# Kernel optimization log

Measured on AMD Instinct MI355X. Metric: run time of the kernel, lower is better.

Reference implementation:

```python
import jax, jax.numpy as jnp
import numpy as np

B, T, C, H, W = 16, 8, 2048, 16, 8
C8, C4, HW, NP = C // 8, C // 4, H * W, T // 2


def _cbr(x, w, s, b):
    # 1x1 conv + folded BN (eval-mode affine) + ReLU; x: (N, Cin, H, W), w: (Cout, Cin)
    y = jnp.einsum('oc,nchw->nohw', w, x)
    return jax.nn.relu(y * s[None, :, None, None] + b[None, :, None, None])


def setup_inputs():
    key = jax.random.key(0)
    ks = jax.random.split(key, 16)
    r = lambda i, shape, sc: jax.random.normal(ks[i], shape, jnp.float32) * sc
    return dict(
        featmap=r(0, (B, T, C, H, W), 1.0),
        re_featmap=r(1, (B * T, C, H, W), 1.0),
        vect_featmap=r(2, (B, T, C), 1.0),
        embed_feat=r(3, (B, T, 128, H, W), 1.0),
        gamma_w=r(4, (C8, C), 0.03), gamma_s=jnp.ones((C8,)), gamma_b=jnp.zeros((C8,)),
        beta_w=r(5, (C8, C), 0.03), beta_s=jnp.ones((C8,)), beta_b=jnp.zeros((C8,)),
        gg_w=r(6, (128, 2 * HW), 0.05), gg_s=jnp.ones((128,)), gg_b=jnp.zeros((128,)),
        tte_w=r(7, (128, 256), 0.05), tte_s=jnp.ones((128,)), tte_b=jnp.zeros((128,)),
        te_w=r(8, (1, 256), 0.05), te_s=jnp.ones((1,)), te_b=jnp.zeros((1,)),
        theta_w=r(9, (C8, C), 0.03), theta_b=jnp.zeros((C8,)),
        cp_w1=r(10, (C8, C4), 0.05), cp_b1=jnp.zeros((C8,)),
        cp_w2=r(11, (C, C8), 0.05), cp_b2=jnp.zeros((C,)),
    )


def reference(featmap, re_featmap, vect_featmap, embed_feat,
              gamma_w, gamma_s, gamma_b, beta_w, beta_s, beta_b,
              gg_w, gg_s, gg_b, tte_w, tte_s, tte_b, te_w, te_s, te_b,
              theta_w, theta_b, cp_w1, cp_b1, cp_w2, cp_b2):
    # spatial attention embeddings: (B, T, C8, HW)
    gamma = _cbr(re_featmap, gamma_w, gamma_s, gamma_b).reshape(B, T, C8, HW)
    beta = _cbr(re_featmap, beta_w, beta_s, beta_b).reshape(B, T, C8, HW)

    # channel attention: Conv1d over time of (B, C, T) -> (B, C8, T)
    cp = jax.nn.relu(jnp.einsum('oc,btc->bot', theta_w, vect_featmap) + theta_b[None, :, None])
    cp = cp.reshape(B, C8, NP, 2)
    c0 = cp[..., 0].transpose(0, 2, 1)  # (B, NP, C8)
    c1 = cp[..., 1].transpose(0, 2, 1)

    def mlp(x):  # (B, NP, C4) -> sigmoid gate (B, NP, C)
        h1 = jax.nn.relu(x @ cp_w1.T + cp_b1)
        return jax.nn.sigmoid(h1 @ cp_w2.T + cp_b2)

    p00 = mlp(jnp.concatenate([c0, c1], -1))  # (B, NP, C)
    p01 = mlp(jnp.concatenate([c1, c0], -1))

    # pairwise spatial graphs
    g0, g1 = gamma[:, 0::2], gamma[:, 1::2]  # (B, NP, C8, HW)
    b0, b1 = beta[:, 0::2], beta[:, 1::2]
    Gs0 = jnp.einsum('bpcs,bpct->bpst', g0, b1)  # (B, NP, HW, HW)
    Gs1 = jnp.einsum('bpcs,bpct->bpst', g1, b0)
    # Gs_in = Gs^T viewed as (HW, H, W); Gs_out = Gs viewed likewise
    j0 = jnp.concatenate([Gs0.transpose(0, 1, 3, 2), Gs1], 2).reshape(B * NP, 2 * HW, H, W)
    j1 = jnp.concatenate([Gs1.transpose(0, 1, 3, 2), Gs0], 2).reshape(B * NP, 2 * HW, H, W)
    gj0 = _cbr(j0, gg_w, gg_s, gg_b)  # (B*NP, 128, H, W)
    gj1 = _cbr(j1, gg_w, gg_s, gg_b)

    ef = embed_feat.reshape(B, NP, 2, 128, H, W)
    e0 = ef[:, :, 0].reshape(B * NP, 128, H, W)
    e1 = ef[:, :, 1].reshape(B * NP, 128, H, W)
    ta = _cbr(jnp.concatenate([e0, e1], 1), tte_w, tte_s, tte_b)  # (B*NP, 128, H, W)
    tb = _cbr(jnp.concatenate([e1, e0], 1), tte_w, tte_s, tte_b)

    def gate(t_feat, gj):  # conv 256->1 + BN + sigmoid
        y = jnp.einsum('oc,nchw->nohw', te_w, jnp.concatenate([t_feat, gj], 1))
        return jax.nn.sigmoid(y * te_s[None, :, None, None] + te_b[None, :, None, None])

    pa = gate(ta, gj0).reshape(B, NP, 1, H, W)
    pb = gate(tb, gj1).reshape(B, NP, 1, H, W)

    f = featmap.reshape(B, NP, 2, C, H, W)
    gate0 = p00[..., None, None] * pa  # (B, NP, C, H, W)
    gate1 = p01[..., None, None] * pb
    out = jax.nn.relu(gate0 * f[:, :, 0] + gate1 * f[:, :, 1])
    return out * out  # (B, T//2, C, H, W)
```

## Files before the change

### kernel.cpp

```cpp
#include <hip/hip_runtime.h>
#include <stdint.h>


typedef _Float16 f16;
typedef _Float16 f16x4 __attribute__((ext_vector_type(4)));
typedef _Float16 f16x8 __attribute__((ext_vector_type(8)));
typedef float f32x4 __attribute__((ext_vector_type(4)));

typedef const void __attribute__((address_space(1)))* gptr1;
typedef void __attribute__((address_space(3)))* lptr3;

__device__ __forceinline__ void gload16(const void* g, void* l) {
  __builtin_amdgcn_global_load_lds((gptr1)g, (lptr3)l, 16, 0, 0);
}

__device__ __forceinline__ float sigmoidf_(float x) { return 1.f / (1.f + expf(-x)); }

#define WAIT_VM6 asm volatile("s_waitcnt vmcnt(6)" ::: "memory")
#define WAIT_VM0 asm volatile("s_waitcnt vmcnt(0)" ::: "memory")
#define WAIT_LGKM8 asm volatile("s_waitcnt lgkmcnt(8)" ::: "memory")
#define WAIT_LGKM0 asm volatile("s_waitcnt lgkmcnt(0)" ::: "memory")

__global__ __launch_bounds__(256) void kPP(const float* __restrict__ x,
                                           f16* __restrict__ Af,
                                           const float* __restrict__ gw, const float* __restrict__ gs,
                                           const float* __restrict__ bw, const float* __restrict__ bs,
                                           const float* __restrict__ gg_w, const float* __restrict__ gg_s,
                                           const float* __restrict__ tte_w, const float* __restrict__ tte_s,
                                           const float* __restrict__ thw, const float* __restrict__ w1,
                                           const float* __restrict__ w2,
                                           f16* __restrict__ Wf,
                                           float* __restrict__ ggT, float* __restrict__ tteT,
                                           float* __restrict__ thwT, float* __restrict__ w1T,
                                           float* __restrict__ w2T) {
  __shared__ __align__(16) char shmem[64 * 65 * 4];
  int t = threadIdx.x;
  int bid = blockIdx.x;
  if (bid < 8192) {
    float (*L)[65] = (float(*)[65])shmem;
    int n = bid >> 6;
    int kc = (bid >> 1) & 31;
    int hh = bid & 1;
    int k0 = kc * 64;
    const float* src = x + (size_t)n * 262144 + (size_t)k0 * 128 + hh * 64;
    for (int r = 0; r < 4; ++r) {
      int f = r * 256 + t;
      int kk = f >> 4, c4 = (f & 15) * 4;
      float4 v = *(const float4*)(src + (size_t)kk * 128 + c4);
      L[kk][c4 + 0] = v.x; L[kk][c4 + 1] = v.y; L[kk][c4 + 2] = v.z; L[kk][c4 + 3] = v.w;
    }
    __syncthreads();
    for (int r = 0; r < 2; ++r) {
      int id = r * 256 + t;
      int hw = id >> 3, c = id & 7;
      int cs = c ^ (hw & 7);
      f16x8 h8;
      for (int j = 0; j < 8; ++j)
        h8[j] = (f16)L[cs * 8 + j][hw];
      size_t m = (size_t)n * 128 + hh * 64 + hw;
      size_t ob = m * 2048 + (size_t)k0 + (size_t)c * 8;
      *(f16x8*)(Af + ob) = h8;
    }
    return;
  }
  if (bid < 8704) {
    int id = (bid - 8192) * 256 + t;
    int o = id >> 8, cch = id & 255;
    float s; const float* row;
    if (o < 256) { s = gs[o]; row = gw + (size_t)o * 2048; }
    else         { s = bs[o - 256]; row = bw + (size_t)(o - 256) * 2048; }
    int kb = cch >> 3, sub = cch & 7;
    int subd = sub ^ (o & 7);
    f16x8 h8;
    for (int j = 0; j < 8; ++j)
      h8[j] = (f16)(row[cch * 8 + j] * s);
    size_t ob = (size_t)o * 2048 + (size_t)kb * 64 + (size_t)subd * 8;
    *(f16x8*)(Wf + ob) = h8;
    return;
  }
  float (*TL)[65] = (float(*)[65])shmem;
  int tb = bid - 8704;
  const float* src; float* dst; const float* scale = nullptr; int R, C;
  if (tb < 128)      { src = thw;   dst = thwT; R = 256;  C = 2048; }
  else if (tb < 256) { tb -= 128; src = w2;  dst = w2T;  R = 2048; C = 256; }
  else if (tb < 288) { tb -= 256; src = w1;  dst = w1T;  R = 256;  C = 512; }
  else if (tb < 296) { tb -= 288; src = gg_w;  dst = ggT;  scale = gg_s;  R = 128; C = 256; }
  else               { tb -= 296; src = tte_w; dst = tteT; scale = tte_s; R = 128; C = 256; }
  int tpc = C >> 6;
  int r0 = (tb / tpc) * 64, c0 = (tb % tpc) * 64;
  int i16 = t >> 4, j4 = (t & 15) * 4;
  for (int s = 0; s < 4; ++s) {
    int i = i16 + s * 16;
    float4 v = *(const float4*)(src + (size_t)(r0 + i) * C + c0 + j4);
    TL[i][j4 + 0] = v.x; TL[i][j4 + 1] = v.y; TL[i][j4 + 2] = v.z; TL[i][j4 + 3] = v.w;
  }
  __syncthreads();
  for (int s = 0; s < 4; ++s) {
    int j = i16 + s * 16;
    float4 w;
    w.x = TL[j4 + 0][j]; w.y = TL[j4 + 1][j]; w.z = TL[j4 + 2][j]; w.w = TL[j4 + 3][j];
    if (scale) {
      w.x *= scale[r0 + j4 + 0]; w.y *= scale[r0 + j4 + 1];
      w.z *= scale[r0 + j4 + 2]; w.w *= scale[r0 + j4 + 3];
    }
    *(float4*)(dst + (size_t)(c0 + j) * R + r0 + j4) = w;
  }
}

__global__ __launch_bounds__(512, 2) void kGemm8(const f16* __restrict__ Af, const f16* __restrict__ Wf,
                                                 const float* __restrict__ gamma_b, const float* __restrict__ beta_b,
                                                 f16* __restrict__ gammaFh, f16* __restrict__ betaFh) {
  __shared__ __align__(16) f16 S[3][24576];
  int t = threadIdx.x;
  int lane = t & 63, wid = t >> 6;
  int wr = wid >> 2, wc = wid & 3;
  int bid = blockIdx.x;
  int bx = (bid & 7) * 16 + (bid >> 4);
  int by = (bid >> 3) & 1;
  size_t M0 = (size_t)bx * 128;
  size_t N0 = (size_t)by * 256;
  int row8 = wid * 8 + (lane >> 3);
  int sl = lane & 7;
  int fr = lane & 15, fq = lane >> 4;
  f32x4 acc[4][4] = {};
  f16x8 a[8], b[8];

  const char* AB = (const char*)Af;
  const char* WB = (const char*)Wf;
  const size_t aoff0 = (M0 + row8) * 4096 + (size_t)sl * 16;
  const size_t aoff1 = (M0 + 64 + row8) * 4096 + (size_t)sl * 16;
  const size_t woff0 = (N0 + row8) * 4096 + (size_t)sl * 16;
  const size_t woff1 = (N0 + 64 + row8) * 4096 + (size_t)sl * 16;
  const size_t woff2 = (N0 + 128 + row8) * 4096 + (size_t)sl * 16;
  const size_t woff3 = (N0 + 192 + row8) * 4096 + (size_t)sl * 16;

#define STAGE_ALL(dst, s) do {                                                     \
    int koff_ = (s) << 7;                                                          \
    char* l_ = (char*)(dst) + wid * 1024;                                          \
    gload16(AB + aoff0 + koff_, l_);                                               \
    gload16(AB + aoff1 + koff_, l_ + 8192);                                        \
    gload16(WB + woff0 + koff_, l_ + 16384);                                       \
    gload16(WB + woff1 + koff_, l_ + 24576);                                       \
    gload16(WB + woff2 + koff_, l_ + 32768);                                       \
    gload16(WB + woff3 + koff_, l_ + 40960);                                       \
  } while (0)

#define LOADG(buf, g) do {                                                         \
    const f16* bA_ = (const f16*)(buf);                                            \
    const f16* bB_ = bA_ + 8192;                                                   \
    int cg_ = (g) * 4 + fq;                                                        \
    _Pragma("unroll") for (int mi = 0; mi < 4; ++mi) {                             \
      int m_ = wr * 64 + mi * 16 + fr;                                             \
      a[(g) * 4 + mi] = *(const f16x8*)(bA_ + m_ * 64 + ((cg_ ^ (m_ & 7)) << 3));  \
    }                                                                              \
    _Pragma("unroll") for (int ni = 0; ni < 4; ++ni) {                             \
      int n_ = wc * 64 + ni * 16 + fr;                                             \
      b[(g) * 4 + ni] = *(const f16x8*)(bB_ + n_ * 64 + ((cg_ ^ (n_ & 7)) << 3));  \
    }                                                                              \
  } while (0)

#define STEP(rdbuf, stbuf, kt) do {                                                \
    if ((kt) < 31) { WAIT_VM6; } else { WAIT_VM0; }                                \
    __builtin_amdgcn_s_barrier();                                                  \
    if ((kt) <= 29) STAGE_ALL(stbuf, (kt) + 2);                                    \
    LOADG(rdbuf, 0);                                                               \
    __builtin_amdgcn_sched_barrier(0);                                             \
    LOADG(rdbuf, 1);                                                               \
    WAIT_LGKM8;                                                                    \
    __builtin_amdgcn_sched_barrier(0);                                             \
    __builtin_amdgcn_s_setprio(1);                                                 \
    _Pragma("unroll") for (int mi = 0; mi < 4; ++mi)                               \
      _Pragma("unroll") for (int ni = 0; ni < 4; ++ni)                             \
        acc[mi][ni] = __builtin_amdgcn_mfma_f32_16x16x32_f16(a[mi], b[ni], acc[mi][ni], 0, 0, 0); \
    WAIT_LGKM0;                                                                    \
    __builtin_amdgcn_sched_barrier(0);                                             \
    _Pragma("unroll") for (int mi = 0; mi < 4; ++mi)                               \
      _Pragma("unroll") for (int ni = 0; ni < 4; ++ni)                             \
        acc[mi][ni] = __builtin_amdgcn_mfma_f32_16x16x32_f16(a[4 + mi], b[4 + ni], acc[mi][ni], 0, 0, 0); \
    __builtin_amdgcn_s_setprio(0);                                                 \
  } while (0)

  STAGE_ALL(&S[0][0], 0);
  STAGE_ALL(&S[1][0], 1);
  for (int base = 0; base < 30; base += 3) {
    STEP(&S[0][0], &S[2][0], base);
    STEP(&S[1][0], &S[0][0], base + 1);
    STEP(&S[2][0], &S[1][0], base + 2);
  }
  STEP(&S[0][0], &S[2][0], 30);
  STEP(&S[1][0], &S[0][0], 31);
#undef STEP
#undef LOADG
#undef STAGE_ALL

  const float* bias = by ? beta_b : gamma_b;
  f16* outb = by ? betaFh : gammaFh;
#pragma unroll
  for (int mi = 0; mi < 4; ++mi) {
    int hwb = wr * 64 + mi * 16 + fq * 4;
#pragma unroll
    for (int ni = 0; ni < 4; ++ni) {
      int o = wc * 64 + ni * 16 + fr;
      float bb = bias[o];
      f32x4 v = acc[mi][ni];
      f16x4 w;
      w[0] = (f16)fmaxf(v[0] + bb, 0.f);
      w[1] = (f16)fmaxf(v[1] + bb, 0.f);
      w[2] = (f16)fmaxf(v[2] + bb, 0.f);
      w[3] = (f16)fmaxf(v[3] + bb, 0.f);
      *(f16x4*)(outb + (size_t)bx * 32768 + (size_t)o * 128 + hwb) = w;
    }
  }
}

__global__ __launch_bounds__(256) void kTT(const float* __restrict__ vect, const float* __restrict__ thwT,
                                           float* __restrict__ P,
                                           const float* __restrict__ embed, const float* __restrict__ tteT,
                                           const float* __restrict__ tte_b, const float* __restrict__ te_w,
                                           float* __restrict__ Sta) {
  __shared__ float V[512];
  __shared__ __align__(16) float E[256 * 64];
  __shared__ float Red[16 * 64];
  int bid = blockIdx.x;
  int t = threadIdx.x;
  if (bid < 512) {
    int bt = bid & 127, kq = bid >> 7;
    const float* src = vect + (size_t)bt * 2048 + kq * 512;
    if (t < 128) *(float4*)(V + t * 4) = *(const float4*)(src + t * 4);
    __syncthreads();
    const float* wp = thwT + (size_t)kq * 512 * 256 + t;
    float acc = 0.f;
#pragma unroll 8
    for (int c = 0; c < 512; ++c)
      acc = fmaf(wp[(size_t)c * 256], V[c], acc);
    P[((size_t)kq * 128 + bt) * 256 + t] = acc;
    return;
  }
  int i = bid - 512;
  int n = i & 63, gate = (i >> 6) & 1, hh = (i >> 7) & 1;
  int b = n >> 2, p = n & 3;
  const float* eA = embed + (size_t)(b * 8 + 2 * p + gate) * 16384 + hh * 64;
  const float* eB = embed + (size_t)(b * 8 + 2 * p + 1 - gate) * 16384 + hh * 64;
  for (int r = 0; r < 8; ++r) {
    int f = r * 256 + t;
    int ch = f >> 4, q = (f & 15) * 4;
    *(float4*)(E + ch * 64 + q) = *(const float4*)(eA + (size_t)ch * 128 + q);
  }
  for (int r = 0; r < 8; ++r) {
    int f = r * 256 + t;
    int ch = f >> 4, q = (f & 15) * 4;
    *(float4*)(E + (128 + ch) * 64 + q) = *(const float4*)(eB + (size_t)ch * 128 + q);
  }
  __syncthreads();
  int ty = t >> 4, tx = t & 15;
  float acc[8][4] = {};
  for (int c = 0; c < 256; ++c) {
    float w8[8];
    *(float4*)w8 = *(const float4*)(tteT + (size_t)c * 128 + ty * 8);
    *(float4*)(w8 + 4) = *(const float4*)(tteT + (size_t)c * 128 + ty * 8 + 4);
    float4 g = *(const float4*)(E + c * 64 + tx * 4);
    for (int ii = 0; ii < 8; ++ii) {
      acc[ii][0] = fmaf(w8[ii], g.x, acc[ii][0]);
      acc[ii][1] = fmaf(w8[ii], g.y, acc[ii][1]);
      acc[ii][2] = fmaf(w8[ii], g.z, acc[ii][2]);
      acc[ii][3] = fmaf(w8[ii], g.w, acc[ii][3]);
    }
  }
  float par[4] = {0.f, 0.f, 0.f, 0.f};
  for (int ii = 0; ii < 8; ++ii) {
    int o = ty * 8 + ii;
    float tb = tte_b[o], tw = te_w[o];
    for (int j = 0; j < 4; ++j)
      par[j] += tw * fmaxf(acc[ii][j] + tb, 0.f);
  }
  for (int j = 0; j < 4; ++j) Red[ty * 64 + tx * 4 + j] = par[j];
  __syncthreads();
  if (t < 64) {
    float s = 0.f;
    for (int g = 0; g < 16; ++g) s += Red[g * 64 + t];
    Sta[(size_t)gate * 8192 + n * 128 + hh * 64 + t] = s;
  }
}

__global__ __launch_bounds__(256) void kAG(const float* __restrict__ P, const float* __restrict__ thb,
                                           const float* __restrict__ w1T, const float* __restrict__ b1,
                                           float* __restrict__ h1,
                                           const f16* __restrict__ gammaFh, const f16* __restrict__ betaFh,
                                           float* __restrict__ Gs0, float* __restrict__ Gs1) {
  __shared__ float x0[256], x1[256];
  __shared__ float ra[256], rb[256];
  __shared__ __align__(16) float As[16 * 128];
  __shared__ __align__(16) float Bs[16 * 64];
  int bid = blockIdx.x;
  int t = threadIdx.x;
  if (bid < 256) {
    int bp = bid & 63, och = bid >> 6;
    int b = bp >> 2, p = bp & 3;
    int bt0 = b * 8 + 2 * p, bt1 = bt0 + 1;
    {
      float a0 = 0.f, a1 = 0.f;
      for (int q = 0; q < 4; ++q) {
        a0 += P[((size_t)q * 128 + bt0) * 256 + t];
        a1 += P[((size_t)q * 128 + bt1) * 256 + t];
      }
      float tb = thb[t];
      x0[t] = fmaxf(a0 + tb, 0.f);
      x1[t] = fmaxf(a1 + tb, 0.f);
    }
    __syncthreads();
    int o = och * 64 + (t & 63);
    int ks = t >> 6;
    const float* xa = (ks < 2) ? x0 : x1;
    const float* xb = (ks < 2) ? x1 : x0;
    int kbase = ks * 128;
    int xoff = (ks < 2) ? kbase : kbase - 256;
    float aa = 0.f, ab = 0.f;
#pragma unroll 8
    for (int ii = 0; ii < 128; ++ii) {
      float w = w1T[(size_t)(kbase + ii) * 256 + o];
      aa = fmaf(w, xa[xoff + ii], aa);
      ab = fmaf(w, xb[xoff + ii], ab);
    }
    ra[t] = aa;
    rb[t] = ab;
    __syncthreads();
    if (t < 64) {
      float sa = ra[t] + ra[64 + t] + ra[128 + t] + ra[192 + t];
      float sb = rb[t] + rb[64 + t] + rb[128 + t] + rb[192 + t];
      float bb = b1[o];
      h1[((size_t)bp * 2) * 256 + o] = fmaxf(sa + bb, 0.f);
      h1[((size_t)bp * 2 + 1) * 256 + o] = fmaxf(sb + bb, 0.f);
    }
    return;
  }
  int i = bid - 256;
  int n = i & 63, which = (i >> 6) & 1, th = (i >> 7) & 1;
  int b = n >> 2, p = n & 3;
  int tg = 2 * p + which;
  int tb = 2 * p + 1 - which;
  const f16* A = gammaFh + (size_t)(b * 8 + tg) * 32768;
  const f16* Bm = betaFh + (size_t)(b * 8 + tb) * 32768;
  float* out = (which ? Gs1 : Gs0) + (size_t)n * 16384;
  int ty = t >> 4, tx = t & 15;
  float acc[8][4] = {};
  for (int c0 = 0; c0 < 256; c0 += 16) {
    {
      int cc = t >> 4, col8 = (t & 15) * 8;
      f16x8 v = *(const f16x8*)(A + (size_t)(c0 + cc) * 128 + col8);
      for (int j = 0; j < 8; ++j) As[cc * 128 + col8 + j] = (float)v[j];
    }
    if (t < 128) {
      int cc = t >> 3, col8 = (t & 7) * 8;
      f16x8 v = *(const f16x8*)(Bm + (size_t)(c0 + cc) * 128 + th * 64 + col8);
      for (int j = 0; j < 8; ++j) Bs[cc * 64 + col8 + j] = (float)v[j];
    }
    __syncthreads();
    for (int cc = 0; cc < 16; ++cc) {
      float a8[8];
      *(float4*)a8 = *(const float4*)(As + cc * 128 + ty * 8);
      *(float4*)(a8 + 4) = *(const float4*)(As + cc * 128 + ty * 8 + 4);
      float4 b4 = *(const float4*)(Bs + cc * 64 + tx * 4);
      for (int ii = 0; ii < 8; ++ii) {
        acc[ii][0] = fmaf(a8[ii], b4.x, acc[ii][0]);
        acc[ii][1] = fmaf(a8[ii], b4.y, acc[ii][1]);
        acc[ii][2] = fmaf(a8[ii], b4.z, acc[ii][2]);
        acc[ii][3] = fmaf(a8[ii], b4.w, acc[ii][3]);
      }
    }
    __syncthreads();
  }
  for (int ii = 0; ii < 8; ++ii) {
    *(float4*)(out + (size_t)(ty * 8 + ii) * 128 + th * 64 + tx * 4) =
        make_float4(acc[ii][0], acc[ii][1], acc[ii][2], acc[ii][3]);
  }
}

__global__ __launch_bounds__(256) void kBG(const float* __restrict__ h1, const float* __restrict__ w2T,
                                           const float* __restrict__ b2,
                                           float* __restrict__ p00, float* __restrict__ p01,
                                           const float* __restrict__ Gs0, const float* __restrict__ Gs1,
                                           const float* __restrict__ ggT, const float* __restrict__ gg_b,
                                           const float* __restrict__ te_w, float* __restrict__ Sgj) {
  __shared__ float ha[256], hb[256];
  __shared__ float G0h[64 * 129];
  __shared__ __align__(16) float G1c[128 * 64];
  __shared__ float Red[16 * 64];
  int bid = blockIdx.x;
  int t = threadIdx.x;
  if (bid < 512) {
    int bp = bid & 63, chc = bid >> 6;
    ha[t] = h1[((size_t)bp * 2) * 256 + t];
    hb[t] = h1[((size_t)bp * 2 + 1) * 256 + t];
    __syncthreads();
    int ch = chc * 256 + t;
    float sa = 0.f, sb = 0.f;
#pragma unroll 8
    for (int k = 0; k < 256; ++k) {
      float w = w2T[(size_t)k * 2048 + ch];
      sa = fmaf(w, ha[k], sa);
      sb = fmaf(w, hb[k], sb);
    }
    p00[(size_t)bp * 2048 + ch] = sigmoidf_(sa + b2[ch]);
    p01[(size_t)bp * 2048 + ch] = sigmoidf_(sb + b2[ch]);
    return;
  }
  int i = bid - 512;
  int n = i & 63, gate = (i >> 6) & 1, hh = (i >> 7) & 1;
  const float* srcT = (gate == 0 ? Gs0 : Gs1) + (size_t)n * 16384;
  const float* srcC = (gate == 0 ? Gs1 : Gs0) + (size_t)n * 16384;
  for (int r = 0; r < 8; ++r) {
    int f = r * 256 + t;
    int hwl = f >> 5, c4 = (f & 31) * 4;
    float4 v = *(const float4*)(srcT + (size_t)(hh * 64 + hwl) * 128 + c4);
    G0h[hwl * 129 + c4 + 0] = v.x;
    G0h[hwl * 129 + c4 + 1] = v.y;
    G0h[hwl * 129 + c4 + 2] = v.z;
    G0h[hwl * 129 + c4 + 3] = v.w;
  }
  for (int r = 0; r < 8; ++r) {
    int f = r * 256 + t;
    int c = f >> 4, q = (f & 15) * 4;
    *(float4*)(G1c + c * 64 + q) = *(const float4*)(srcC + (size_t)c * 128 + hh * 64 + q);
  }
  __syncthreads();
  int ty = t >> 4, tx = t & 15;
  float acc[8][4] = {};
  for (int c = 0; c < 128; ++c) {
    float w8[8];
    *(float4*)w8 = *(const float4*)(ggT + (size_t)c * 128 + ty * 8);
    *(float4*)(w8 + 4) = *(const float4*)(ggT + (size_t)c * 128 + ty * 8 + 4);
    float g4[4];
    for (int j = 0; j < 4; ++j) g4[j] = G0h[(tx * 4 + j) * 129 + c];
    for (int ii = 0; ii < 8; ++ii)
      for (int j = 0; j < 4; ++j)
        acc[ii][j] = fmaf(w8[ii], g4[j], acc[ii][j]);
  }
  for (int c = 0; c < 128; ++c) {
    float w8[8];
    *(float4*)w8 = *(const float4*)(ggT + (size_t)(128 + c) * 128 + ty * 8);
    *(float4*)(w8 + 4) = *(const float4*)(ggT + (size_t)(128 + c) * 128 + ty * 8 + 4);
    float4 g = *(const float4*)(G1c + c * 64 + tx * 4);
    for (int ii = 0; ii < 8; ++ii) {
      acc[ii][0] = fmaf(w8[ii], g.x, acc[ii][0]);
      acc[ii][1] = fmaf(w8[ii], g.y, acc[ii][1]);
      acc[ii][2] = fmaf(w8[ii], g.z, acc[ii][2]);
      acc[ii][3] = fmaf(w8[ii], g.w, acc[ii][3]);
    }
  }
  float par[4] = {0.f, 0.f, 0.f, 0.f};
  for (int ii = 0; ii < 8; ++ii) {
    int o = ty * 8 + ii;
    float gb = gg_b[o], tw = te_w[128 + o];
    for (int j = 0; j < 4; ++j)
      par[j] += tw * fmaxf(acc[ii][j] + gb, 0.f);
  }
  for (int j = 0; j < 4; ++j) Red[ty * 64 + tx * 4 + j] = par[j];
  __syncthreads();
  if (t < 64) {
    float s = 0.f;
    for (int g = 0; g < 16; ++g) s += Red[g * 64 + t];
    Sgj[(size_t)gate * 8192 + n * 128 + hh * 64 + t] = s;
  }
}

__global__ __launch_bounds__(256) void kFinal(const float* __restrict__ featmap, const float* __restrict__ p00,
                                              const float* __restrict__ p01, const float* __restrict__ Sta,
                                              const float* __restrict__ Sgj, const float* __restrict__ te_s,
                                              const float* __restrict__ te_b, float* __restrict__ out) {
  int fid = blockIdx.x * 256 + threadIdx.x;
  int h4 = (fid & 31) * 4;
  int c = (fid >> 5) & 2047;
  int bp = fid >> 16;
  int b = bp >> 2, p = bp & 3;
  float ga = p00[(size_t)bp * 2048 + c];
  float gb = p01[(size_t)bp * 2048 + c];
  float ts = te_s[0], tbv = te_b[0];
  float4 sa0 = *(const float4*)(Sta + (size_t)bp * 128 + h4);
  float4 sg0 = *(const float4*)(Sgj + (size_t)bp * 128 + h4);
  float4 sa1 = *(const float4*)(Sta + 8192 + (size_t)bp * 128 + h4);
  float4 sg1 = *(const float4*)(Sgj + 8192 + (size_t)bp * 128 + h4);
  float4 pa4, pb4;
  pa4.x = sigmoidf_(ts * (sa0.x + sg0.x) + tbv);
  pa4.y = sigmoidf_(ts * (sa0.y + sg0.y) + tbv);
  pa4.z = sigmoidf_(ts * (sa0.z + sg0.z) + tbv);
  pa4.w = sigmoidf_(ts * (sa0.w + sg0.w) + tbv);
  pb4.x = sigmoidf_(ts * (sa1.x + sg1.x) + tbv);
  pb4.y = sigmoidf_(ts * (sa1.y + sg1.y) + tbv);
  pb4.z = sigmoidf_(ts * (sa1.z + sg1.z) + tbv);
  pb4.w = sigmoidf_(ts * (sa1.w + sg1.w) + tbv);
  const float* f0 = featmap + (size_t)(b * 8 + 2 * p) * 262144 + (size_t)c * 128 + h4;
  const float* f1 = f0 + 262144;
  float4 v0 = *(const float4*)f0;
  float4 v1 = *(const float4*)f1;
  float4 o4;
  float r;
  r = fmaxf(ga * pa4.x * v0.x + gb * pb4.x * v1.x, 0.f); o4.x = r * r;
  r = fmaxf(ga * pa4.y * v0.y + gb * pb4.y * v1.y, 0.f); o4.y = r * r;
  r = fmaxf(ga * pa4.z * v0.z + gb * pb4.z * v1.z, 0.f); o4.z = r * r;
  r = fmaxf(ga * pa4.w * v0.w + gb * pb4.w * v1.w, 0.f); o4.w = r * r;
  *(float4*)(out + (size_t)fid * 4) = o4;
}

extern "C" void kernel_launch(void* const* d_in, const int* in_sizes, int n_in,
                              void* d_out, int out_size, void* d_ws, size_t ws_size,
                              hipStream_t stream) {
  (void)in_sizes; (void)n_in; (void)out_size; (void)ws_size;
  const float* featmap    = (const float*)d_in[0];
  const float* re_featmap = (const float*)d_in[1];
  const float* vect       = (const float*)d_in[2];
  const float* embed      = (const float*)d_in[3];
  const float* gamma_w    = (const float*)d_in[4];
  const float* gamma_s    = (const float*)d_in[5];
  const float* gamma_b    = (const float*)d_in[6];
  const float* beta_w     = (const float*)d_in[7];
  const float* beta_s     = (const float*)d_in[8];
  const float* beta_b     = (const float*)d_in[9];
  const float* gg_w       = (const float*)d_in[10];
  const float* gg_s       = (const float*)d_in[11];
  const float* gg_b       = (const float*)d_in[12];
  const float* tte_w      = (const float*)d_in[13];
  const float* tte_s      = (const float*)d_in[14];
  const float* tte_b      = (const float*)d_in[15];
  const float* te_w       = (const float*)d_in[16];
  const float* te_s       = (const float*)d_in[17];
  const float* te_b       = (const float*)d_in[18];
  const float* theta_w    = (const float*)d_in[19];
  const float* theta_b    = (const float*)d_in[20];
  const float* cp_w1      = (const float*)d_in[21];
  const float* cp_b1      = (const float*)d_in[22];
  const float* cp_w2      = (const float*)d_in[23];
  const float* cp_b2      = (const float*)d_in[24];
  float* out = (float*)d_out;

  char* w = (char*)d_ws;
  f16* Af  = (f16*)w;   w += (size_t)16384 * 2048 * 2;
  f16* Wf  = (f16*)w;   w += (size_t)512 * 2048 * 2;
  f16* gammaFh = (f16*)w; w += (size_t)128 * 256 * 128 * 2;
  f16* betaFh  = (f16*)w; w += (size_t)128 * 256 * 128 * 2;
  float* Gs0    = (float*)w; w += (size_t)64 * 128 * 128 * 4;
  float* Gs1    = (float*)w; w += (size_t)64 * 128 * 128 * 4;
  float* ggT    = (float*)w; w += (size_t)256 * 128 * 4;
  float* tteT   = (float*)w; w += (size_t)256 * 128 * 4;
  float* thwT   = (float*)w; w += (size_t)2048 * 256 * 4;
  float* w1T    = (float*)w; w += (size_t)512 * 256 * 4;
  float* w2T    = (float*)w; w += (size_t)256 * 2048 * 4;
  float* P      = (float*)w; w += (size_t)4 * 128 * 256 * 4;
  float* h1     = (float*)w; w += (size_t)64 * 2 * 256 * 4;
  float* Sta    = (float*)w; w += (size_t)2 * 64 * 128 * 4;
  float* Sgj    = (float*)w; w += (size_t)2 * 64 * 128 * 4;
  float* p00    = (float*)w; w += (size_t)64 * 2048 * 4;
  float* p01    = (float*)w; w += (size_t)64 * 2048 * 4;

  kPP<<<9008, 256, 0, stream>>>(re_featmap, Af,
                                gamma_w, gamma_s, beta_w, beta_s, gg_w, gg_s, tte_w, tte_s,
                                theta_w, cp_w1, cp_w2, Wf, ggT, tteT, thwT, w1T, w2T);
  kGemm8<<<256, 512, 0, stream>>>(Af, Wf, gamma_b, beta_b, gammaFh, betaFh);
  kTT<<<768, 256, 0, stream>>>(vect, thwT, P, embed, tteT, tte_b, te_w, Sta);
  kAG<<<512, 256, 0, stream>>>(P, theta_b, w1T, cp_b1, h1, gammaFh, betaFh, Gs0, Gs1);
  kBG<<<768, 256, 0, stream>>>(h1, w2T, cp_b2, p00, p01, Gs0, Gs1, ggT, gg_b, te_w, Sgj);
  kFinal<<<16384, 256, 0, stream>>>(featmap, p00, p01, Sta, Sgj, te_s, te_b, out);
}
```

Baseline: 248.3 us.

## Fuse activation transpose and fp16 conversion into GEMM A-operand loading

The separate pre-pass that transposed re_featmap into an fp16 (M,K) buffer is removed. The GEMM now reads fp32 activations directly into registers, converts them to fp16 and writes them swizzled into LDS inside its pipelined K loop, while the weights still stream via direct global-to-LDS loads. This drops a full write and re-read of a 64 MB intermediate, at the cost of more register pressure and VALU/LDS-store work inside the GEMM main loop.

```diff
diff --git a/kernel.cpp b/kernel.cpp
--- a/kernel.cpp
+++ b/kernel.cpp
@@ -3,6 +3,7 @@
 
 
 typedef _Float16 f16;
+typedef _Float16 f16x2 __attribute__((ext_vector_type(2)));
 typedef _Float16 f16x4 __attribute__((ext_vector_type(4)));
 typedef _Float16 f16x8 __attribute__((ext_vector_type(8)));
 typedef float f32x4 __attribute__((ext_vector_type(4)));
@@ -16,14 +17,14 @@
 
 __device__ __forceinline__ float sigmoidf_(float x) { return 1.f / (1.f + expf(-x)); }
 
-#define WAIT_VM6 asm volatile("s_waitcnt vmcnt(6)" ::: "memory")
+#define WAIT_VM8 asm volatile("s_waitcnt vmcnt(8)" ::: "memory")
 #define WAIT_VM0 asm volatile("s_waitcnt vmcnt(0)" ::: "memory")
 #define WAIT_LGKM8 asm volatile("s_waitcnt lgkmcnt(8)" ::: "memory")
 #define WAIT_LGKM0 asm volatile("s_waitcnt lgkmcnt(0)" ::: "memory")
-
-__global__ __launch_bounds__(256) void kPP(const float* __restrict__ x,
-                                           f16* __restrict__ Af,
-                                           const float* __restrict__ gw, const float* __restrict__ gs,
+#define SBAR __builtin_amdgcn_s_barrier()
+#define SCHED0 __builtin_amdgcn_sched_barrier(0)
+
+__global__ __launch_bounds__(256) void kPP(const float* __restrict__ gw, const float* __restrict__ gs,
                                            const float* __restrict__ bw, const float* __restrict__ bs,
                                            const float* __restrict__ gg_w, const float* __restrict__ gg_s,
                                            const float* __restrict__ tte_w, const float* __restrict__ tte_s,
@@ -33,38 +34,11 @@
                                            float* __restrict__ ggT, float* __restrict__ tteT,
                                            float* __restrict__ thwT, float* __restrict__ w1T,
                                            float* __restrict__ w2T) {
-  __shared__ __align__(16) char shmem[64 * 65 * 4];
+  __shared__ __align__(16) float TL[64][65];
   int t = threadIdx.x;
   int bid = blockIdx.x;
-  if (bid < 8192) {
-    float (*L)[65] = (float(*)[65])shmem;
-    int n = bid >> 6;
-    int kc = (bid >> 1) & 31;
-    int hh = bid & 1;
-    int k0 = kc * 64;
-    const float* src = x + (size_t)n * 262144 + (size_t)k0 * 128 + hh * 64;
-    for (int r = 0; r < 4; ++r) {
-      int f = r * 256 + t;
-      int kk = f >> 4, c4 = (f & 15) * 4;
-      float4 v = *(const float4*)(src + (size_t)kk * 128 + c4);
-      L[kk][c4 + 0] = v.x; L[kk][c4 + 1] = v.y; L[kk][c4 + 2] = v.z; L[kk][c4 + 3] = v.w;
-    }
-    __syncthreads();
-    for (int r = 0; r < 2; ++r) {
-      int id = r * 256 + t;
-      int hw = id >> 3, c = id & 7;
-      int cs = c ^ (hw & 7);
-      f16x8 h8;
-      for (int j = 0; j < 8; ++j)
-        h8[j] = (f16)L[cs * 8 + j][hw];
-      size_t m = (size_t)n * 128 + hh * 64 + hw;
-      size_t ob = m * 2048 + (size_t)k0 + (size_t)c * 8;
-      *(f16x8*)(Af + ob) = h8;
-    }
-    return;
-  }
-  if (bid < 8704) {
-    int id = (bid - 8192) * 256 + t;
+  if (bid < 512) {
+    int id = bid * 256 + t;
     int o = id >> 8, cch = id & 255;
     float s; const float* row;
     if (o < 256) { s = gs[o]; row = gw + (size_t)o * 2048; }
@@ -78,8 +52,7 @@
     *(f16x8*)(Wf + ob) = h8;
     return;
   }
-  float (*TL)[65] = (float(*)[65])shmem;
-  int tb = bid - 8704;
+  int tb = bid - 512;
   const float* src; float* dst; const float* scale = nullptr; int R, C;
   if (tb < 128)      { src = thw;   dst = thwT; R = 256;  C = 2048; }
   else if (tb < 256) { tb -= 128; src = w2;  dst = w2T;  R = 2048; C = 256; }
@@ -107,7 +80,7 @@
   }
 }
 
-__global__ __launch_bounds__(512, 2) void kGemm8(const f16* __restrict__ Af, const f16* __restrict__ Wf,
+__global__ __launch_bounds__(512, 2) void kGemm8(const float* __restrict__ X, const f16* __restrict__ Wf,
                                                  const float* __restrict__ gamma_b, const float* __restrict__ beta_b,
                                                  f16* __restrict__ gammaFh, f16* __restrict__ betaFh) {
   __shared__ __align__(16) f16 S[3][24576];
@@ -117,32 +90,64 @@
   int bid = blockIdx.x;
   int bx = (bid & 7) * 16 + (bid >> 4);
   int by = (bid >> 3) & 1;
-  size_t M0 = (size_t)bx * 128;
   size_t N0 = (size_t)by * 256;
   int row8 = wid * 8 + (lane >> 3);
   int sl = lane & 7;
   int fr = lane & 15, fq = lane >> 4;
   f32x4 acc[4][4] = {};
   f16x8 a[8], b[8];
-
-  const char* AB = (const char*)Af;
+  float4 ar0[4], ar1[4];
+
+  const float* Xb = X + (size_t)bx * 262144;
+  int kkB = 2 * ((lane >> 3) + ((wid >> 2) << 3));
+  int hw4 = ((lane & 7) << 2) + ((wid & 3) << 5);
+  int wo[2][4];
+#pragma unroll
+  for (int r = 0; r < 2; ++r) {
+    int kk = kkB + 32 * r;
+    int cg = kk >> 3, kp = kk & 7;
+#pragma unroll
+    for (int j = 0; j < 4; ++j) {
+      int hw = hw4 + j;
+      wo[r][j] = hw * 64 + ((cg ^ (hw & 7)) << 3) + kp;
+    }
+  }
+
   const char* WB = (const char*)Wf;
-  const size_t aoff0 = (M0 + row8) * 4096 + (size_t)sl * 16;
-  const size_t aoff1 = (M0 + 64 + row8) * 4096 + (size_t)sl * 16;
   const size_t woff0 = (N0 + row8) * 4096 + (size_t)sl * 16;
   const size_t woff1 = (N0 + 64 + row8) * 4096 + (size_t)sl * 16;
   const size_t woff2 = (N0 + 128 + row8) * 4096 + (size_t)sl * 16;
   const size_t woff3 = (N0 + 192 + row8) * 4096 + (size_t)sl * 16;
 
-#define STAGE_ALL(dst, s) do {                                                     \
+#define AISSUE(bank, s) do {                                                       \
+    const float* p_ = Xb + ((s) * 64 + kkB) * 128 + hw4;                           \
+    bank[0] = *(const float4*)(p_);                                                \
+    bank[1] = *(const float4*)(p_ + 128);                                          \
+    bank[2] = *(const float4*)(p_ + 4096);                                         \
+    bank[3] = *(const float4*)(p_ + 4096 + 128);                                   \
+  } while (0)
+
+#define WSTAGE(dst, s) do {                                                        \
     int koff_ = (s) << 7;                                                          \
-    char* l_ = (char*)(dst) + wid * 1024;                                          \
-    gload16(AB + aoff0 + koff_, l_);                                               \
-    gload16(AB + aoff1 + koff_, l_ + 8192);                                        \
-    gload16(WB + woff0 + koff_, l_ + 16384);                                       \
-    gload16(WB + woff1 + koff_, l_ + 24576);                                       \
-    gload16(WB + woff2 + koff_, l_ + 32768);                                       \
-    gload16(WB + woff3 + koff_, l_ + 40960);                                       \
+    char* l_ = (char*)(dst) + 16384 + wid * 1024;                                  \
+    gload16(WB + woff0 + koff_, l_);                                               \
+    gload16(WB + woff1 + koff_, l_ + 8192);                                        \
+    gload16(WB + woff2 + koff_, l_ + 16384);                                       \
+    gload16(WB + woff3 + koff_, l_ + 24576);                                       \
+  } while (0)
+
+#define AWRITE(bank, dst) do {                                                     \
+    f16* ad_ = (f16*)(dst);                                                        \
+    _Pragma("unroll") for (int r_ = 0; r_ < 2; ++r_) {                             \
+      const float* lo_ = (const float*)&bank[2 * r_];                              \
+      const float* hi_ = (const float*)&bank[2 * r_ + 1];                          \
+      _Pragma("unroll") for (int j_ = 0; j_ < 4; ++j_) {                           \
+        f16x2 h_;                                                                  \
+        h_[0] = (f16)lo_[j_];                                                      \
+        h_[1] = (f16)hi_[j_];                                                      \
+        *(f16x2*)(ad_ + wo[r_][j_]) = h_;                                          \
+      }                                                                            \
+    }                                                                              \
   } while (0)
 
 #define LOADG(buf, g) do {                                                         \
@@ -159,39 +164,59 @@
     }                                                                              \
   } while (0)
 
-#define STEP(rdbuf, stbuf, kt) do {                                                \
-    if ((kt) < 31) { WAIT_VM6; } else { WAIT_VM0; }                                \
-    __builtin_amdgcn_s_barrier();                                                  \
-    if ((kt) <= 29) STAGE_ALL(stbuf, (kt) + 2);                                    \
-    LOADG(rdbuf, 0);                                                               \
-    __builtin_amdgcn_sched_barrier(0);                                             \
-    LOADG(rdbuf, 1);                                                               \
-    WAIT_LGKM8;                                                                    \
-    __builtin_amdgcn_sched_barrier(0);                                             \
-    __builtin_amdgcn_s_setprio(1);                                                 \
+#define MFMA_G(g) do {                                                             \
     _Pragma("unroll") for (int mi = 0; mi < 4; ++mi)                               \
       _Pragma("unroll") for (int ni = 0; ni < 4; ++ni)                             \
-        acc[mi][ni] = __builtin_amdgcn_mfma_f32_16x16x32_f16(a[mi], b[ni], acc[mi][ni], 0, 0, 0); \
+        acc[mi][ni] = __builtin_amdgcn_mfma_f32_16x16x32_f16(                      \
+            a[(g) * 4 + mi], b[(g) * 4 + ni], acc[mi][ni], 0, 0, 0);               \
+  } while (0)
+
+#define STEP(cur, nxt, n2, s, BI, BW) do {                                         \
+    SBAR;                                                                          \
+    if ((s) <= 29) { AISSUE(BI, (s) + 2); WSTAGE(n2, (s) + 2); }                   \
+    SCHED0;                                                                        \
+    if ((s) <= 29) { WAIT_VM8; } else { WAIT_VM0; }                                \
+    SCHED0;                                                                        \
+    if ((s) <= 30) AWRITE(BW, nxt);                                                \
+    SCHED0;                                                                        \
+    LOADG(cur, 0);                                                                 \
+    SCHED0;                                                                        \
+    LOADG(cur, 1);                                                                 \
+    WAIT_LGKM8;                                                                    \
+    SCHED0;                                                                        \
+    __builtin_amdgcn_s_setprio(1);                                                 \
+    MFMA_G(0);                                                                     \
     WAIT_LGKM0;                                                                    \
-    __builtin_amdgcn_sched_barrier(0);                                             \
-    _Pragma("unroll") for (int mi = 0; mi < 4; ++mi)                               \
-      _Pragma("unroll") for (int ni = 0; ni < 4; ++ni)                             \
-        acc[mi][ni] = __builtin_amdgcn_mfma_f32_16x16x32_f16(a[4 + mi], b[4 + ni], acc[mi][ni], 0, 0, 0); \
+    SCHED0;                                                                        \
+    MFMA_G(1);                                                                     \
     __builtin_amdgcn_s_setprio(0);                                                 \
   } while (0)
 
-  STAGE_ALL(&S[0][0], 0);
-  STAGE_ALL(&S[1][0], 1);
-  for (int base = 0; base < 30; base += 3) {
-    STEP(&S[0][0], &S[2][0], base);
-    STEP(&S[1][0], &S[0][0], base + 1);
-    STEP(&S[2][0], &S[1][0], base + 2);
-  }
-  STEP(&S[0][0], &S[2][0], 30);
-  STEP(&S[1][0], &S[0][0], 31);
+  AISSUE(ar0, 0); WSTAGE(&S[0][0], 0);
+  SCHED0;
+  AISSUE(ar1, 1); WSTAGE(&S[1][0], 1);
+  SCHED0;
+  WAIT_VM8;
+  SCHED0;
+  AWRITE(ar0, &S[0][0]);
+  WAIT_LGKM0;
+
+  for (int base = 0; base < 30; base += 6) {
+    STEP(&S[0][0], &S[1][0], &S[2][0], base + 0, ar0, ar1);
+    STEP(&S[1][0], &S[2][0], &S[0][0], base + 1, ar1, ar0);
+    STEP(&S[2][0], &S[0][0], &S[1][0], base + 2, ar0, ar1);
+    STEP(&S[0][0], &S[1][0], &S[2][0], base + 3, ar1, ar0);
+    STEP(&S[1][0], &S[2][0], &S[0][0], base + 4, ar0, ar1);
+    STEP(&S[2][0], &S[0][0], &S[1][0], base + 5, ar1, ar0);
+  }
+  STEP(&S[0][0], &S[1][0], &S[2][0], 30, ar0, ar1);
+  STEP(&S[1][0], &S[2][0], &S[0][0], 31, ar1, ar0);
 #undef STEP
+#undef MFMA_G
 #undef LOADG
-#undef STAGE_ALL
+#undef AWRITE
+#undef WSTAGE
+#undef AISSUE
 
   const float* bias = by ? beta_b : gamma_b;
   f16* outb = by ? betaFh : gammaFh;
@@ -533,7 +558,6 @@
   float* out = (float*)d_out;
 
   char* w = (char*)d_ws;
-  f16* Af  = (f16*)w;   w += (size_t)16384 * 2048 * 2;
   f16* Wf  = (f16*)w;   w += (size_t)512 * 2048 * 2;
   f16* gammaFh = (f16*)w; w += (size_t)128 * 256 * 128 * 2;
   f16* betaFh  = (f16*)w; w += (size_t)128 * 256 * 128 * 2;
@@ -551,10 +575,9 @@
   float* p00    = (float*)w; w += (size_t)64 * 2048 * 4;
   float* p01    = (float*)w; w += (size_t)64 * 2048 * 4;
 
-  kPP<<<9008, 256, 0, stream>>>(re_featmap, Af,
-                                gamma_w, gamma_s, beta_w, beta_s, gg_w, gg_s, tte_w, tte_s,
-                                theta_w, cp_w1, cp_w2, Wf, ggT, tteT, thwT, w1T, w2T);
-  kGemm8<<<256, 512, 0, stream>>>(Af, Wf, gamma_b, beta_b, gammaFh, betaFh);
+  kPP<<<816, 256, 0, stream>>>(gamma_w, gamma_s, beta_w, beta_s, gg_w, gg_s, tte_w, tte_s,
+                               theta_w, cp_w1, cp_w2, Wf, ggT, tteT, thwT, w1T, w2T);
+  kGemm8<<<256, 512, 0, stream>>>(re_featmap, Wf, gamma_b, beta_b, gammaFh, betaFh);
   kTT<<<768, 256, 0, stream>>>(vect, thwT, P, embed, tteT, tte_b, te_w, Sta);
   kAG<<<512, 256, 0, stream>>>(P, theta_b, w1T, cp_b1, h1, gammaFh, betaFh, Gs0, Gs1);
   kBG<<<768, 256, 0, stream>>>(h1, w2T, cp_b2, p00, p01, Gs0, Gs1, ggT, gg_b, te_w, Sgj);
```

After: 240.1 us. 3.3% less time.
